# Optimization experiments

Measured on AMD Instinct MI355X. Metric: run time of the kernel, lower is better.

The kernel has to match this reference:

```python
import jax, jax.numpy as jnp
import numpy as np

NUM_LEVELS = 8
BASE_RES = 16
MAX_RES = 1024
TABLE_SIZE = 2 ** 17
FEAT = 2
ALPHA_SHIFT = 5.0
ALPHA_SCALE = 1.0

_growth = np.exp((np.log(MAX_RES) - np.log(BASE_RES)) / (NUM_LEVELS - 1))
SCALINGS = np.floor(BASE_RES * _growth ** np.arange(NUM_LEVELS)).astype(np.float32)  # per-level grid res
CORNERS = np.array([[(i >> 2) & 1, (i >> 1) & 1, i & 1] for i in range(8)], dtype=np.int32)  # voxel corners
PRIMES = np.array([1, 2654435761, 805459861], dtype=np.uint32)  # nerfstudio hash primes


def hash_encode(pos, table):
    # pos: [N,3] in [0,1]; table: [NUM_LEVELS*TABLE_SIZE, FEAT]
    scaled = pos[:, None, :] * jnp.asarray(SCALINGS)[None, :, None]              # [N,L,3]
    f = jnp.floor(scaled)
    w = scaled - f                                                               # trilinear weights
    idx = f.astype(jnp.int32)[:, :, None, :] + jnp.asarray(CORNERS)[None, None]  # [N,L,8,3]
    h = idx.astype(jnp.uint32) * jnp.asarray(PRIMES)
    hashed = (h[..., 0] ^ h[..., 1] ^ h[..., 2]) % TABLE_SIZE                    # [N,L,8]
    hashed = hashed.astype(jnp.int32) + (jnp.arange(NUM_LEVELS, dtype=jnp.int32) * TABLE_SIZE)[None, :, None]
    feats = table[hashed]                                                        # [N,L,8,F] gather
    cw = jnp.where(jnp.asarray(CORNERS)[None, None] == 1, w[:, :, None, :], 1.0 - w[:, :, None, :]).prod(-1)
    out = (feats * cw[..., None]).sum(2)                                         # [N,L,F]
    return out.reshape(pos.shape[0], NUM_LEVELS * FEAT)


def setup_inputs():
    key = jax.random.key(0)
    ks = jax.random.split(key, 8)
    R, S = 8192, 48
    return {
        "positions": jax.random.normal(ks[0], (R, S, 3), jnp.float32),
        "c2ws": jax.random.normal(ks[1], (R, 3, 4), jnp.float32) * 0.5,
        "aabb": jnp.array([[-1.0, -1.0, -1.0], [1.0, 1.0, 1.0]], jnp.float32),
        "table": jax.random.uniform(ks[2], (NUM_LEVELS * TABLE_SIZE, FEAT), jnp.float32, -1e-4, 1e-4),
        "w1": jax.random.normal(ks[3], (16, 32), jnp.float32) * 0.25,
        "b1": jnp.zeros((32,), jnp.float32),
        "w2": jax.random.normal(ks[4], (32, 16), jnp.float32) * 0.18,
        "b2": jnp.zeros((16,), jnp.float32),
        "hw1": jax.random.normal(ks[5], (16, 64), jnp.float32) * 0.25,
        "hb1": jnp.zeros((64,), jnp.float32),
        "hw2": jax.random.normal(ks[6], (64, 1), jnp.float32) * 0.125,
        "hb2": jnp.zeros((1,), jnp.float32),
    }


def reference(positions, c2ws, aabb, table, w1, b1, w2, b2, hw1, hb1, hw2, hb2):
    R, S = positions.shape[:2]
    rot = c2ws[:, :3, :3]
    trans = c2ws[:, :3, 3]
    rot_t = jnp.swapaxes(rot, 1, 2)                          # w2c rotation = R^T
    t_w2c = -jnp.einsum('rij,rj->ri', rot_t, trans)          # w2c translation = -R^T t
    pos = jnp.einsum('rij,rsj->rsi', rot_t, positions) + t_w2c[:, None, :]
    pos = (pos - aabb[0]) / (aabb[1] - aabb[0])              # SceneBox.get_normalized_positions
    selector = jnp.all((pos > 0.0) & (pos < 1.0), axis=-1)   # inside unit cube
    pos = pos * selector[..., None]
    enc = hash_encode(pos.reshape(-1, 3), table)             # [N, 16]
    h = jax.nn.relu(enc @ w1 + b1) @ w2 + b2                 # mlp_base -> geo features
    o = jax.nn.relu(h @ hw1 + hb1) @ hw2 + hb2               # mlp_head -> alpha logits
    o = o.reshape(R, S, -1)
    return ALPHA_SCALE * jax.nn.sigmoid(o - ALPHA_SHIFT) * selector[..., None]
```

## Files before the change

### kernel.cpp

```cpp
#include <hip/hip_runtime.h>
#include <math.h>
#include <stdint.h>

#define NLEV 8
#define TSIZE 131072
#define TMASK (TSIZE - 1)

__device__ __forceinline__ void transform_pos(
    const float* __restrict__ positions, const float* __restrict__ c2ws,
    const float* __restrict__ aabb, int gid, int S,
    float& posx, float& posy, float& posz, bool& sel)
{
    int r = gid / S;
    const float* p = positions + (size_t)gid * 3;
    const float* c = c2ws + (size_t)r * 12;
    float px = __builtin_nontemporal_load(p + 0);
    float py = __builtin_nontemporal_load(p + 1);
    float pz = __builtin_nontemporal_load(p + 2);
    float c00 = c[0], c01 = c[1], c02 = c[2],  t0 = c[3];
    float c10 = c[4], c11 = c[5], c12 = c[6],  t1 = c[7];
    float c20 = c[8], c21 = c[9], c22 = c[10], t2 = c[11];

    float m0 = __fadd_rn(__fadd_rn(__fmul_rn(c00, px), __fmul_rn(c10, py)), __fmul_rn(c20, pz));
    float m1 = __fadd_rn(__fadd_rn(__fmul_rn(c01, px), __fmul_rn(c11, py)), __fmul_rn(c21, pz));
    float m2 = __fadd_rn(__fadd_rn(__fmul_rn(c02, px), __fmul_rn(c12, py)), __fmul_rn(c22, pz));
    float n0 = __fadd_rn(__fadd_rn(__fmul_rn(c00, t0), __fmul_rn(c10, t1)), __fmul_rn(c20, t2));
    float n1 = __fadd_rn(__fadd_rn(__fmul_rn(c01, t0), __fmul_rn(c11, t1)), __fmul_rn(c21, t2));
    float n2 = __fadd_rn(__fadd_rn(__fmul_rn(c02, t0), __fmul_rn(c12, t1)), __fmul_rn(c22, t2));
    float x0 = __fsub_rn(m0, n0);
    float x1 = __fsub_rn(m1, n1);
    float x2 = __fsub_rn(m2, n2);

    float a0x = aabb[0], a0y = aabb[1], a0z = aabb[2];
    float a1x = aabb[3], a1y = aabb[4], a1z = aabb[5];
    posx = __fdiv_rn(__fsub_rn(x0, a0x), __fsub_rn(a1x, a0x));
    posy = __fdiv_rn(__fsub_rn(x1, a0y), __fsub_rn(a1y, a0y));
    posz = __fdiv_rn(__fsub_rn(x2, a0z), __fsub_rn(a1z, a0z));
    sel = (posx > 0.f) & (posx < 1.f) & (posy > 0.f) & (posy < 1.f) & (posz > 0.f) & (posz < 1.f);
}

__global__ __launch_bounds__(256) void rif_encode_lm(
    const float* __restrict__ positions,
    const float* __restrict__ c2ws,
    const float* __restrict__ aabb,
    const float* __restrict__ table,
    float* __restrict__ out,
    float* __restrict__ encbuf,
    int total, int S)
{
    int g     = blockIdx.x & 3;
    int chunk = blockIdx.x >> 2;
    int half  = threadIdx.x >> 7;
    int sl    = threadIdx.x & 127;
    int gid   = chunk * 128 + sl;
    if (gid >= total) return;
    int l = half ? (7 - g) : g;

    float posx, posy, posz; bool sel;
    transform_pos(positions, c2ws, aabb, gid, S, posx, posy, posz, sel);
    if (!sel) {
        if (g == 0 && half == 0) __builtin_nontemporal_store(0.f, out + gid);
        return;
    }

    float sc = (l == 0) ? 16.f : (l == 1) ? 28.f : (l == 2) ? 52.f : (l == 3) ? 95.f
             : (l == 4) ? 172.f : (l == 5) ? 312.f : (l == 6) ? 565.f : 1024.f;

    float sx = posx * sc, sy = posy * sc, sz = posz * sc;
    float fx = floorf(sx), fy = floorf(sy), fz = floorf(sz);
    float wx = sx - fx, wy = sy - fy, wz = sz - fz;
    uint32_t ix = (uint32_t)(int)fx, iy = (uint32_t)(int)fy, iz = (uint32_t)(int)fz;
    uint32_t hy0 = iy * 2654435761u, hy1 = hy0 + 2654435761u;
    uint32_t hz0 = iz * 805459861u,  hz1 = hz0 + 805459861u;
    const float2* tab = (const float2*)table + (size_t)l * TSIZE;

    float2 ft[8];
    #pragma unroll
    for (int cc = 0; cc < 8; ++cc) {
        uint32_t cx = (cc >> 2) & 1, cy = (cc >> 1) & 1, cz = cc & 1;
        uint32_t hh = ((ix + cx) ^ (cy ? hy1 : hy0) ^ (cz ? hz1 : hz0)) & TMASK;
        ft[cc] = tab[hh];
    }
    __builtin_amdgcn_sched_barrier(0);

    float ux = 1.f - wx, uy = 1.f - wy, uz = 1.f - wz;
    float q00 = uy * uz, q01 = uy * wz, q10 = wy * uz, q11 = wy * wz;
    float f0, f1;
    f0 = ft[0].x * (ux * q00); f1 = ft[0].y * (ux * q00);
    f0 = fmaf(ft[1].x, ux * q01, f0); f1 = fmaf(ft[1].y, ux * q01, f1);
    f0 = fmaf(ft[2].x, ux * q10, f0); f1 = fmaf(ft[2].y, ux * q10, f1);
    f0 = fmaf(ft[3].x, ux * q11, f0); f1 = fmaf(ft[3].y, ux * q11, f1);
    f0 = fmaf(ft[4].x, wx * q00, f0); f1 = fmaf(ft[4].y, wx * q00, f1);
    f0 = fmaf(ft[5].x, wx * q01, f0); f1 = fmaf(ft[5].y, wx * q01, f1);
    f0 = fmaf(ft[6].x, wx * q10, f0); f1 = fmaf(ft[6].y, wx * q10, f1);
    f0 = fmaf(ft[7].x, wx * q11, f0); f1 = fmaf(ft[7].y, wx * q11, f1);

    __builtin_nontemporal_store(f0, encbuf + (size_t)(2 * l) * total + gid);
    __builtin_nontemporal_store(f1, encbuf + (size_t)(2 * l + 1) * total + gid);
}

__global__ __launch_bounds__(256, 2) void rif_mlp(
    const float* __restrict__ positions,
    const float* __restrict__ c2ws,
    const float* __restrict__ aabb,
    const float* __restrict__ w1, const float* __restrict__ b1,
    const float* __restrict__ w2, const float* __restrict__ b2,
    const float* __restrict__ hw1, const float* __restrict__ hb1,
    const float* __restrict__ hw2, const float* __restrict__ hb2,
    float* __restrict__ out,
    const float* __restrict__ encbuf,
    int total, int S)
{
    __shared__ int sIdx[256];
    __shared__ int wbase[4];
    __shared__ int sCnt;

    int gid = blockIdx.x * 256 + threadIdx.x;
    bool sel = false;
    if (gid < total) {
        float posx, posy, posz;
        transform_pos(positions, c2ws, aabb, gid, S, posx, posy, posz, sel);
    }

    unsigned long long m = __ballot(sel);
    int lane = threadIdx.x & 63;
    int wid  = threadIdx.x >> 6;
    int pre  = __popcll(m & ((1ull << lane) - 1ull));
    if (lane == 0) wbase[wid] = __popcll(m);
    __syncthreads();
    if (threadIdx.x == 0) {
        int s = 0;
        #pragma unroll
        for (int w = 0; w < 4; ++w) { int t = wbase[w]; wbase[w] = s; s += t; }
        sCnt = s;
    }
    __syncthreads();
    if (sel) sIdx[wbase[wid] + pre] = threadIdx.x;
    __syncthreads();

    int cnt = sCnt;
    int t = threadIdx.x;
    if (t >= cnt) return;
    int ogid = blockIdx.x * 256 + sIdx[t];

    float enc[16];
    #pragma unroll
    for (int j = 0; j < 16; ++j) enc[j] = encbuf[(size_t)j * total + ogid];

    float h1[32];
    #pragma unroll
    for (int j = 0; j < 32; ++j) h1[j] = b1[j];
    #pragma unroll
    for (int i = 0; i < 16; ++i) {
        float e = enc[i];
        #pragma unroll
        for (int j = 0; j < 32; ++j) h1[j] = fmaf(e, w1[i * 32 + j], h1[j]);
    }
    #pragma unroll
    for (int j = 0; j < 32; ++j) h1[j] = fmaxf(h1[j], 0.f);

    float h2[16];
    #pragma unroll
    for (int j = 0; j < 16; ++j) h2[j] = b2[j];
    #pragma unroll
    for (int i = 0; i < 32; ++i) {
        float e = h1[i];
        #pragma unroll
        for (int j = 0; j < 16; ++j) h2[j] = fmaf(e, w2[i * 16 + j], h2[j]);
    }

    float o = hb2[0];
    #pragma unroll
    for (int j = 0; j < 64; ++j) {
        float acc = hb1[j];
        #pragma unroll
        for (int i = 0; i < 16; ++i) acc = fmaf(h2[i], hw1[i * 64 + j], acc);
        o = fmaf(fmaxf(acc, 0.f), hw2[j], o);
    }

    float x = o - 5.0f;
    out[ogid] = 1.0f / (1.0f + expf(-x));
}

__global__ __launch_bounds__(256, 2) void rif_fused(
    const float* __restrict__ positions,
    const float* __restrict__ c2ws,
    const float* __restrict__ aabb,
    const float* __restrict__ table,
    const float* __restrict__ w1, const float* __restrict__ b1,
    const float* __restrict__ w2, const float* __restrict__ b2,
    const float* __restrict__ hw1, const float* __restrict__ hb1,
    const float* __restrict__ hw2, const float* __restrict__ hb2,
    float* __restrict__ out, int total, int S)
{
    int gid = blockIdx.x * 256 + threadIdx.x;
    if (gid >= total) return;
    float posx, posy, posz; bool sel;
    transform_pos(positions, c2ws, aabb, gid, S, posx, posy, posz, sel);
    if (!sel) { out[gid] = 0.f; return; }

    const float kScale[8] = {16.f, 28.f, 52.f, 95.f, 172.f, 312.f, 565.f, 1024.f};
    float enc[16];
    #pragma unroll
    for (int l = 0; l < NLEV; ++l) {
        float sc = kScale[l];
        float sx = posx * sc, sy = posy * sc, sz = posz * sc;
        float fx = floorf(sx), fy = floorf(sy), fz = floorf(sz);
        float wx = sx - fx, wy = sy - fy, wz = sz - fz;
        uint32_t ix = (uint32_t)(int)fx, iy = (uint32_t)(int)fy, iz = (uint32_t)(int)fz;
        uint32_t hy0 = iy * 2654435761u, hy1 = hy0 + 2654435761u;
        uint32_t hz0 = iz * 805459861u,  hz1 = hz0 + 805459861u;
        const float2* tab = (const float2*)table + (size_t)l * TSIZE;
        float f0 = 0.f, f1 = 0.f;
        #pragma unroll
        for (int cc = 0; cc < 8; ++cc) {
            uint32_t cx = (cc >> 2) & 1, cy = (cc >> 1) & 1, cz = cc & 1;
            uint32_t hh = ((ix + cx) ^ (cy ? hy1 : hy0) ^ (cz ? hz1 : hz0)) & TMASK;
            float wgt = (cx ? wx : 1.f - wx) * (cy ? wy : 1.f - wy) * (cz ? wz : 1.f - wz);
            float2 ftv = tab[hh];
            f0 = fmaf(ftv.x, wgt, f0);
            f1 = fmaf(ftv.y, wgt, f1);
        }
        enc[2 * l] = f0;
        enc[2 * l + 1] = f1;
    }

    float h1[32];
    #pragma unroll
    for (int j = 0; j < 32; ++j) h1[j] = b1[j];
    #pragma unroll
    for (int i = 0; i < 16; ++i) {
        float e = enc[i];
        #pragma unroll
        for (int j = 0; j < 32; ++j) h1[j] = fmaf(e, w1[i * 32 + j], h1[j]);
    }
    #pragma unroll
    for (int j = 0; j < 32; ++j) h1[j] = fmaxf(h1[j], 0.f);

    float h2[16];
    #pragma unroll
    for (int j = 0; j < 16; ++j) h2[j] = b2[j];
    #pragma unroll
    for (int i = 0; i < 32; ++i) {
        float e = h1[i];
        #pragma unroll
        for (int j = 0; j < 16; ++j) h2[j] = fmaf(e, w2[i * 16 + j], h2[j]);
    }

    float o = hb2[0];
    #pragma unroll
    for (int j = 0; j < 64; ++j) {
        float acc = hb1[j];
        #pragma unroll
        for (int i = 0; i < 16; ++i) acc = fmaf(h2[i], hw1[i * 64 + j], acc);
        o = fmaf(fmaxf(acc, 0.f), hw2[j], o);
    }

    float x = o - 5.0f;
    out[gid] = 1.0f / (1.0f + expf(-x));
}

extern "C" void kernel_launch(void* const* d_in, const int* in_sizes, int n_in,
                              void* d_out, int out_size, void* d_ws, size_t ws_size,
                              hipStream_t stream) {
    const float* positions = (const float*)d_in[0];
    const float* c2ws      = (const float*)d_in[1];
    const float* aabb      = (const float*)d_in[2];
    const float* table     = (const float*)d_in[3];
    const float* w1  = (const float*)d_in[4];
    const float* b1  = (const float*)d_in[5];
    const float* w2  = (const float*)d_in[6];
    const float* b2  = (const float*)d_in[7];
    const float* hw1 = (const float*)d_in[8];
    const float* hb1 = (const float*)d_in[9];
    const float* hw2 = (const float*)d_in[10];
    const float* hb2 = (const float*)d_in[11];

    int R = in_sizes[1] / 12;
    int total = in_sizes[0] / 3;
    int S = total / R;

    size_t needed = (size_t)16 * (size_t)total * sizeof(float);
    if (ws_size >= needed) {
        float* encbuf = (float*)d_ws;
        int nchunks = (total + 127) / 128;
        hipLaunchKernelGGL(rif_encode_lm, dim3(nchunks * 4), dim3(256), 0, stream,
                           positions, c2ws, aabb, table,
                           (float*)d_out, encbuf, total, S);
        int blocks2 = (total + 255) / 256;
        hipLaunchKernelGGL(rif_mlp, dim3(blocks2), dim3(256), 0, stream,
                           positions, c2ws, aabb,
                           w1, b1, w2, b2, hw1, hb1, hw2, hb2,
                           (float*)d_out, encbuf, total, S);
    } else {
        int blocks = (total + 255) / 256;
        hipLaunchKernelGGL(rif_fused, dim3(blocks), dim3(256), 0, stream,
                           positions, c2ws, aabb, table,
                           w1, b1, w2, b2, hw1, hb1, hw2, hb2,
                           (float*)d_out, total, S);
    }
}
```

Before: 82.44 us.

## Split position transform into its own kernel and use point-major encoding buffer

Adds a rif_xform kernel that computes the normalized positions and the inside-box mask once and stores them as float4, so the encode and MLP kernels no longer redo the camera transform (previously done 2x in encode, once in MLP). The encoding buffer changes from level-major to point-major, so the MLP reads 16 features as four float4 loads, and the stream compaction in the MLP kernel is removed in favour of an early exit. The cost is a third launch, an extra workspace round-trip for pos4, and scattered float2 stores in the encode kernel. Non-temporal hints are dropped, and inactive lanes in the MLP kernel now sit idle instead of being compacted away.

```diff
diff --git a/kernel.cpp b/kernel.cpp
--- a/kernel.cpp
+++ b/kernel.cpp
@@ -6,17 +6,20 @@
 #define TSIZE 131072
 #define TMASK (TSIZE - 1)
 
-__device__ __forceinline__ void transform_pos(
-    const float* __restrict__ positions, const float* __restrict__ c2ws,
-    const float* __restrict__ aabb, int gid, int S,
-    float& posx, float& posy, float& posz, bool& sel)
+__global__ __launch_bounds__(256) void rif_xform(
+    const float* __restrict__ positions,
+    const float* __restrict__ c2ws,
+    const float* __restrict__ aabb,
+    float* __restrict__ out,
+    float4* __restrict__ pos4,
+    int total, int S)
 {
+    int gid = blockIdx.x * 256 + threadIdx.x;
+    if (gid >= total) return;
     int r = gid / S;
     const float* p = positions + (size_t)gid * 3;
     const float* c = c2ws + (size_t)r * 12;
-    float px = __builtin_nontemporal_load(p + 0);
-    float py = __builtin_nontemporal_load(p + 1);
-    float pz = __builtin_nontemporal_load(p + 2);
+    float px = p[0], py = p[1], pz = p[2];
     float c00 = c[0], c01 = c[1], c02 = c[2],  t0 = c[3];
     float c10 = c[4], c11 = c[5], c12 = c[6],  t1 = c[7];
     float c20 = c[8], c21 = c[9], c22 = c[10], t2 = c[11];
@@ -33,20 +36,20 @@
 
     float a0x = aabb[0], a0y = aabb[1], a0z = aabb[2];
     float a1x = aabb[3], a1y = aabb[4], a1z = aabb[5];
-    posx = __fdiv_rn(__fsub_rn(x0, a0x), __fsub_rn(a1x, a0x));
-    posy = __fdiv_rn(__fsub_rn(x1, a0y), __fsub_rn(a1y, a0y));
-    posz = __fdiv_rn(__fsub_rn(x2, a0z), __fsub_rn(a1z, a0z));
-    sel = (posx > 0.f) & (posx < 1.f) & (posy > 0.f) & (posy < 1.f) & (posz > 0.f) & (posz < 1.f);
-}
-
-__global__ __launch_bounds__(256) void rif_encode_lm(
-    const float* __restrict__ positions,
-    const float* __restrict__ c2ws,
-    const float* __restrict__ aabb,
+    float posx = __fdiv_rn(__fsub_rn(x0, a0x), __fsub_rn(a1x, a0x));
+    float posy = __fdiv_rn(__fsub_rn(x1, a0y), __fsub_rn(a1y, a0y));
+    float posz = __fdiv_rn(__fsub_rn(x2, a0z), __fsub_rn(a1z, a0z));
+    bool sel = (posx > 0.f) & (posx < 1.f) & (posy > 0.f) & (posy < 1.f) & (posz > 0.f) & (posz < 1.f);
+
+    if (!sel) out[gid] = 0.f;
+    pos4[gid] = make_float4(posx, posy, posz, sel ? 1.f : 0.f);
+}
+
+__global__ __launch_bounds__(256) void rif_enc(
+    const float4* __restrict__ pos4,
     const float* __restrict__ table,
-    float* __restrict__ out,
     float* __restrict__ encbuf,
-    int total, int S)
+    int total)
 {
     int g     = blockIdx.x & 3;
     int chunk = blockIdx.x >> 2;
@@ -56,17 +59,13 @@
     if (gid >= total) return;
     int l = half ? (7 - g) : g;
 
-    float posx, posy, posz; bool sel;
-    transform_pos(positions, c2ws, aabb, gid, S, posx, posy, posz, sel);
-    if (!sel) {
-        if (g == 0 && half == 0) __builtin_nontemporal_store(0.f, out + gid);
-        return;
-    }
+    float4 pp = pos4[gid];
+    if (pp.w == 0.f) return;
 
     float sc = (l == 0) ? 16.f : (l == 1) ? 28.f : (l == 2) ? 52.f : (l == 3) ? 95.f
              : (l == 4) ? 172.f : (l == 5) ? 312.f : (l == 6) ? 565.f : 1024.f;
 
-    float sx = posx * sc, sy = posy * sc, sz = posz * sc;
+    float sx = pp.x * sc, sy = pp.y * sc, sz = pp.z * sc;
     float fx = floorf(sx), fy = floorf(sy), fz = floorf(sz);
     float wx = sx - fx, wy = sy - fy, wz = sz - fz;
     uint32_t ix = (uint32_t)(int)fx, iy = (uint32_t)(int)fy, iz = (uint32_t)(int)fz;
@@ -95,57 +94,31 @@
     f0 = fmaf(ft[6].x, wx * q10, f0); f1 = fmaf(ft[6].y, wx * q10, f1);
     f0 = fmaf(ft[7].x, wx * q11, f0); f1 = fmaf(ft[7].y, wx * q11, f1);
 
-    __builtin_nontemporal_store(f0, encbuf + (size_t)(2 * l) * total + gid);
-    __builtin_nontemporal_store(f1, encbuf + (size_t)(2 * l + 1) * total + gid);
+    *(float2*)(encbuf + (size_t)gid * 16 + 2 * l) = make_float2(f0, f1);
 }
 
 __global__ __launch_bounds__(256, 2) void rif_mlp(
-    const float* __restrict__ positions,
-    const float* __restrict__ c2ws,
-    const float* __restrict__ aabb,
+    const float4* __restrict__ pos4,
     const float* __restrict__ w1, const float* __restrict__ b1,
     const float* __restrict__ w2, const float* __restrict__ b2,
     const float* __restrict__ hw1, const float* __restrict__ hb1,
     const float* __restrict__ hw2, const float* __restrict__ hb2,
     float* __restrict__ out,
     const float* __restrict__ encbuf,
-    int total, int S)
+    int total)
 {
-    __shared__ int sIdx[256];
-    __shared__ int wbase[4];
-    __shared__ int sCnt;
-
     int gid = blockIdx.x * 256 + threadIdx.x;
-    bool sel = false;
-    if (gid < total) {
-        float posx, posy, posz;
-        transform_pos(positions, c2ws, aabb, gid, S, posx, posy, posz, sel);
-    }
-
-    unsigned long long m = __ballot(sel);
-    int lane = threadIdx.x & 63;
-    int wid  = threadIdx.x >> 6;
-    int pre  = __popcll(m & ((1ull << lane) - 1ull));
-    if (lane == 0) wbase[wid] = __popcll(m);
-    __syncthreads();
-    if (threadIdx.x == 0) {
-        int s = 0;
-        #pragma unroll
-        for (int w = 0; w < 4; ++w) { int t = wbase[w]; wbase[w] = s; s += t; }
-        sCnt = s;
-    }
-    __syncthreads();
-    if (sel) sIdx[wbase[wid] + pre] = threadIdx.x;
-    __syncthreads();
-
-    int cnt = sCnt;
-    int t = threadIdx.x;
-    if (t >= cnt) return;
-    int ogid = blockIdx.x * 256 + sIdx[t];
+    if (gid >= total) return;
+    if (pos4[gid].w == 0.f) return;
 
     float enc[16];
-    #pragma unroll
-    for (int j = 0; j < 16; ++j) enc[j] = encbuf[(size_t)j * total + ogid];
+    const float4* e4 = (const float4*)(encbuf + (size_t)gid * 16);
+    #pragma unroll
+    for (int q = 0; q < 4; ++q) {
+        float4 v = e4[q];
+        enc[4 * q + 0] = v.x; enc[4 * q + 1] = v.y;
+        enc[4 * q + 2] = v.z; enc[4 * q + 3] = v.w;
+    }
 
     float h1[32];
     #pragma unroll
@@ -179,7 +152,7 @@
     }
 
     float x = o - 5.0f;
-    out[ogid] = 1.0f / (1.0f + expf(-x));
+    out[gid] = 1.0f / (1.0f + expf(-x));
 }
 
 __global__ __launch_bounds__(256, 2) void rif_fused(
@@ -195,8 +168,28 @@
 {
     int gid = blockIdx.x * 256 + threadIdx.x;
     if (gid >= total) return;
-    float posx, posy, posz; bool sel;
-    transform_pos(positions, c2ws, aabb, gid, S, posx, posy, posz, sel);
+    int r = gid / S;
+    const float* p = positions + (size_t)gid * 3;
+    const float* c = c2ws + (size_t)r * 12;
+    float px = p[0], py = p[1], pz = p[2];
+    float c00 = c[0], c01 = c[1], c02 = c[2],  t0 = c[3];
+    float c10 = c[4], c11 = c[5], c12 = c[6],  t1 = c[7];
+    float c20 = c[8], c21 = c[9], c22 = c[10], t2 = c[11];
+    float m0 = __fadd_rn(__fadd_rn(__fmul_rn(c00, px), __fmul_rn(c10, py)), __fmul_rn(c20, pz));
+    float m1 = __fadd_rn(__fadd_rn(__fmul_rn(c01, px), __fmul_rn(c11, py)), __fmul_rn(c21, pz));
+    float m2 = __fadd_rn(__fadd_rn(__fmul_rn(c02, px), __fmul_rn(c12, py)), __fmul_rn(c22, pz));
+    float n0 = __fadd_rn(__fadd_rn(__fmul_rn(c00, t0), __fmul_rn(c10, t1)), __fmul_rn(c20, t2));
+    float n1 = __fadd_rn(__fadd_rn(__fmul_rn(c01, t0), __fmul_rn(c11, t1)), __fmul_rn(c21, t2));
+    float n2 = __fadd_rn(__fadd_rn(__fmul_rn(c02, t0), __fmul_rn(c12, t1)), __fmul_rn(c22, t2));
+    float x0 = __fsub_rn(m0, n0);
+    float x1 = __fsub_rn(m1, n1);
+    float x2 = __fsub_rn(m2, n2);
+    float a0x = aabb[0], a0y = aabb[1], a0z = aabb[2];
+    float a1x = aabb[3], a1y = aabb[4], a1z = aabb[5];
+    float posx = __fdiv_rn(__fsub_rn(x0, a0x), __fsub_rn(a1x, a0x));
+    float posy = __fdiv_rn(__fsub_rn(x1, a0y), __fsub_rn(a1y, a0y));
+    float posz = __fdiv_rn(__fsub_rn(x2, a0z), __fsub_rn(a1z, a0z));
+    bool sel = (posx > 0.f) & (posx < 1.f) & (posy > 0.f) & (posy < 1.f) & (posz > 0.f) & (posz < 1.f);
     if (!sel) { out[gid] = 0.f; return; }
 
     const float kScale[8] = {16.f, 28.f, 52.f, 95.f, 172.f, 312.f, 565.f, 1024.f};
@@ -280,18 +273,24 @@
     int total = in_sizes[0] / 3;
     int S = total / R;
 
-    size_t needed = (size_t)16 * (size_t)total * sizeof(float);
+    size_t enc_bytes  = (size_t)total * 16 * sizeof(float);
+    size_t pos_bytes  = (size_t)total * sizeof(float4);
+    size_t needed = enc_bytes + pos_bytes;
     if (ws_size >= needed) {
-        float* encbuf = (float*)d_ws;
+        float*  encbuf = (float*)d_ws;
+        float4* pos4   = (float4*)((char*)d_ws + enc_bytes);
+
+        int blocks0 = (total + 255) / 256;
+        hipLaunchKernelGGL(rif_xform, dim3(blocks0), dim3(256), 0, stream,
+                           positions, c2ws, aabb, (float*)d_out, pos4, total, S);
+
         int nchunks = (total + 127) / 128;
-        hipLaunchKernelGGL(rif_encode_lm, dim3(nchunks * 4), dim3(256), 0, stream,
-                           positions, c2ws, aabb, table,
-                           (float*)d_out, encbuf, total, S);
-        int blocks2 = (total + 255) / 256;
-        hipLaunchKernelGGL(rif_mlp, dim3(blocks2), dim3(256), 0, stream,
-                           positions, c2ws, aabb,
-                           w1, b1, w2, b2, hw1, hb1, hw2, hb2,
-                           (float*)d_out, encbuf, total, S);
+        hipLaunchKernelGGL(rif_enc, dim3(nchunks * 4), dim3(256), 0, stream,
+                           pos4, table, encbuf, total);
+
+        hipLaunchKernelGGL(rif_mlp, dim3(blocks0), dim3(256), 0, stream,
+                           pos4, w1, b1, w2, b2, hw1, hb1, hw2, hb2,
+                           (float*)d_out, encbuf, total);
     } else {
         int blocks = (total + 255) / 256;
         hipLaunchKernelGGL(rif_fused, dim3(blocks), dim3(256), 0, stream,
```

New measurement: 78.35 us. -5.0%, faster.
